# Performance work log

Measured on AMD Instinct MI355X. Metric: run time of the kernel, lower is better.

The kernel has to match this reference:

```python
import jax, jax.numpy as jnp
import numpy as np
from jax import lax

NUM_GROUPS = 16
POOL_K = 2
CLAMP_MIN = 0.0
CLAMP_MAX = 1.0
EPS = 1e-5


def setup_inputs() -> dict:
    key = jax.random.key(0)
    k1, k2, k3, k4, k5, k6 = jax.random.split(key, 6)
    B, Cin, H, W = 32, 64, 128, 128
    Cout, K = 128, 3
    x = jax.random.normal(k1, (B, Cin, H, W), dtype=jnp.float32)
    conv_w = jax.random.normal(k2, (Cout, Cin, K, K), dtype=jnp.float32) * 0.05
    conv_b = jax.random.normal(k3, (Cout,), dtype=jnp.float32) * 0.05
    gn_weight = jnp.ones((Cout,), dtype=jnp.float32) + 0.1 * jax.random.normal(k4, (Cout,), dtype=jnp.float32)
    gn_bias = 0.1 * jax.random.normal(k5, (Cout,), dtype=jnp.float32)
    scale = jnp.ones((Cout, 1, 1), dtype=jnp.float32) + 0.1 * jax.random.normal(k6, (Cout, 1, 1), dtype=jnp.float32)
    return {"x": x, "conv_w": conv_w, "conv_b": conv_b,
            "gn_weight": gn_weight, "gn_bias": gn_bias, "scale": scale}


def reference(x, conv_w, conv_b, gn_weight, gn_bias, scale):
    # Conv2d, VALID padding, stride 1  -> [B, C, H-2, W-2]
    y = lax.conv_general_dilated(
        x, conv_w, window_strides=(1, 1), padding='VALID',
        dimension_numbers=('NCHW', 'OIHW', 'NCHW'))
    y = y + conv_b[None, :, None, None]

    B, C, H, W = y.shape
    # GroupNorm: stats per (batch, group) over channels_per_group*H*W
    yg = y.reshape(B, NUM_GROUPS, -1)
    mean = jnp.mean(yg, axis=-1, keepdims=True)
    var = jnp.mean(jnp.square(yg - mean), axis=-1, keepdims=True)
    yn = ((yg - mean) * lax.rsqrt(var + EPS)).reshape(B, C, H, W)
    # affine + extra per-channel scale (fused elementwise)
    yn = (yn * gn_weight[None, :, None, None] + gn_bias[None, :, None, None]) * scale[None]

    # MaxPool2d(k=POOL_K), VALID, stride=k
    p = lax.reduce_window(yn, -jnp.inf, lax.max,
                          (1, 1, POOL_K, POOL_K), (1, 1, POOL_K, POOL_K), 'VALID')
    return jnp.clip(p, CLAMP_MIN, CLAMP_MAX)
```

## Files before the change

### kernel.cpp

```cpp
#include <hip/hip_runtime.h>

typedef _Float16 half8 __attribute__((ext_vector_type(8)));
typedef _Float16 half4t __attribute__((ext_vector_type(4)));
typedef _Float16 half2t __attribute__((ext_vector_type(2)));
typedef float float4t __attribute__((ext_vector_type(4)));

#define BATCH 32
#define CIN 64
#define HIN 128
#define WIN 128
#define COUT 128
#define HOUT 126
#define WOUT 126
#define YSTR 128
#define HP 63
#define WP 63
#define NGROUPS 16
#define CPG 8
#define EPSV 1e-5f

__global__ __launch_bounds__(256) void wt_kernel(const float* __restrict__ w,
                                                 _Float16* __restrict__ wT) {
    int idx = blockIdx.x * 256 + threadIdx.x;
    if (idx >= 9 * COUT * CIN) return;
    int cin = idx & 63;
    int t = idx >> 6;
    int cout = t & 127;
    int pos = t >> 7;
    wT[idx] = (_Float16)w[(cout * CIN + cin) * 9 + pos];
}

__global__ __launch_bounds__(256, 3) void conv_mfma_kernel(
    const float* __restrict__ x, const _Float16* __restrict__ wT,
    const float* __restrict__ bias, _Float16* __restrict__ yh,
    float* __restrict__ stats)
{
    __shared__ __align__(16) _Float16 xs[3 * 130 * 64];

    const int tid = threadIdx.x;
    int f = blockIdx.y * 126 + blockIdx.x;
    int w = (f & 7) * 504 + (f >> 3);
    const int oy = w % 126;
    const int b  = w / 126;

    {
        const int cp   = tid & 31;
        const int seg  = tid >> 5;
        const int c0   = 2 * cp;
        const int chk  = cp >> 2;
        const int wsub = (cp & 3) << 1;
        const float* xb = x + (size_t)b * CIN * (HIN * WIN);
        for (int i = 0; i < 12; i++) {
            int r = i >> 2;
            int col4 = seg * 16 + (i & 3) * 4;
            const float* p0 = xb + ((size_t)c0 * HIN + (oy + r)) * WIN + col4;
            const float* p1 = p0 + (size_t)HIN * WIN;
            float4t va = *(const float4t*)p0;
            float4t vb = *(const float4t*)p1;
            int Rb = r * 130 + col4;
#pragma unroll
            for (int j = 0; j < 4; j++) {
                int R = Rb + j;
                half2t hv = { (_Float16)va[j], (_Float16)vb[j] };
                *(half2t*)&xs[(R << 6) + ((chk ^ (R & 7)) << 3) + wsub] = hv;
            }
        }
        if (tid < 192) {
            int cpz = tid & 31;
            int R = (tid >> 6) * 130 + 128 + ((tid >> 5) & 1);
            half2t z = { (_Float16)0.f, (_Float16)0.f };
            *(half2t*)&xs[(R << 6) + (((cpz >> 2) ^ (R & 7)) << 3) + ((cpz & 3) << 1)] = z;
        }
    }
    __syncthreads();

    const int lane = tid & 63;
    const int wv   = tid >> 6;
    const int m    = lane & 15;
    const int q    = lane >> 4;
    const int cout0 = wv * 32;

    float4t acc[2][8];
#pragma unroll
    for (int s = 0; s < 2; s++)
#pragma unroll
        for (int n = 0; n < 8; n++)
            acc[s][n] = (float4t){0.f, 0.f, 0.f, 0.f};

    const _Float16* ab0 = wT + (size_t)(cout0 + m) * CIN + q * 8;
    half8 a0 = *(const half8*)(ab0);
    half8 a1 = *(const half8*)(ab0 + 16 * CIN);

    for (int kk = 0; kk < 18; kk++) {
        int pos = kk >> 1, ch = kk & 1;
        int kh = (pos > 2) + (pos > 5);
        int kw = pos - kh * 3;
        int R0 = kh * 130 + m + kw;
        const _Float16* bb = &xs[(R0 << 6) + (((q + 4 * ch) ^ (R0 & 7)) << 3)];

        half8 na0 = a0, na1 = a1;
        if (kk < 17) {
            int nk = kk + 1, npos = nk >> 1, nch = nk & 1;
            const _Float16* ab = wT + ((size_t)(npos * COUT + cout0 + m)) * CIN + q * 8 + nch * 32;
            na0 = *(const half8*)ab;
            na1 = *(const half8*)(ab + 16 * CIN);
        }
#pragma unroll
        for (int n = 0; n < 8; n++) {
            half8 bf = *(const half8*)(bb + n * 1024);
            acc[0][n] = __builtin_amdgcn_mfma_f32_16x16x32_f16(bf, a0, acc[0][n], 0, 0, 0);
            acc[1][n] = __builtin_amdgcn_mfma_f32_16x16x32_f16(bf, a1, acc[1][n], 0, 0, 0);
        }
        a0 = na0; a1 = na1;
    }

#pragma unroll
    for (int sub = 0; sub < 2; sub++) {
        const int c = cout0 + sub * 16 + m;
        const float bv = bias[c];
        _Float16* yrow = yh + (((size_t)b * COUT + c) * HOUT + oy) * YSTR;
        float sv = 0.f, ssv = 0.f;
#pragma unroll
        for (int n = 0; n < 8; n++) {
            int pix0 = n * 16 + q * 4;
            float v0 = acc[sub][n][0] + bv;
            float v1 = acc[sub][n][1] + bv;
            float v2 = acc[sub][n][2] + bv;
            float v3 = acc[sub][n][3] + bv;
            sv  += v0 + v1;
            ssv += v0 * v0 + v1 * v1;
            if (pix0 + 3 < WOUT) {
                sv  += v2 + v3;
                ssv += v2 * v2 + v3 * v3;
            }
            half4t hv = { (_Float16)v0, (_Float16)v1, (_Float16)v2, (_Float16)v3 };
            *(half4t*)(yrow + pix0) = hv;
        }
        sv  += __shfl_xor(sv, 1);   ssv += __shfl_xor(ssv, 1);
        sv  += __shfl_xor(sv, 2);   ssv += __shfl_xor(ssv, 2);
        sv  += __shfl_xor(sv, 4);   ssv += __shfl_xor(ssv, 4);
        sv  += __shfl_xor(sv, 16);  ssv += __shfl_xor(ssv, 16);
        sv  += __shfl_xor(sv, 32);  ssv += __shfl_xor(ssv, 32);
        if ((lane & 55) == 0) {
            int g = (cout0 >> 3) + sub * 2 + ((lane >> 3) & 1);
            atomicAdd(&stats[(b * NGROUPS + g) * 2 + 0], sv);
            atomicAdd(&stats[(b * NGROUPS + g) * 2 + 1], ssv);
        }
    }
}

__global__ __launch_bounds__(256) void norm_pool_kernel(
    const _Float16* __restrict__ yh, const float* __restrict__ stats,
    const float* __restrict__ gnw, const float* __restrict__ gnb,
    const float* __restrict__ scale, float* __restrict__ out)
{
    int idx = blockIdx.x * 256 + threadIdx.x;
    int wp = idx & 63;
    int hp = (idx >> 6) & 63;
    if (wp >= WP || hp >= HP) return;
    int c  = (idx >> 12) & 127;
    int b  = idx >> 19;

    const float N = (float)(CPG * HOUT * WOUT);
    int g = c >> 3;
    float sum   = stats[(b * NGROUPS + g) * 2 + 0];
    float sumsq = stats[(b * NGROUPS + g) * 2 + 1];
    float mean = sum / N;
    float var  = sumsq / N - mean * mean;
    float rstd = rsqrtf(var + EPSV);

    float gw = gnw[c] * rstd;
    float A  = gw * scale[c];
    float B2 = (gnb[c] - mean * gw) * scale[c];

    const _Float16* yp = yh + ((((size_t)b * COUT + c) * HOUT + hp * 2) << 7) + wp * 2;
    half2t r0 = *(const half2t*)yp;
    half2t r1 = *(const half2t*)(yp + YSTR);
    float v0 = fmaf((float)r0[0], A, B2);
    float v1 = fmaf((float)r0[1], A, B2);
    float v2 = fmaf((float)r1[0], A, B2);
    float v3 = fmaf((float)r1[1], A, B2);
    float mx = fmaxf(fmaxf(v0, v1), fmaxf(v2, v3));
    out[(((size_t)b * COUT + c) * HP + hp) * WP + wp] = fminf(fmaxf(mx, 0.0f), 1.0f);
}

extern "C" void kernel_launch(void* const* d_in, const int* in_sizes, int n_in,
                              void* d_out, int out_size, void* d_ws, size_t ws_size,
                              hipStream_t stream) {
    const float* x      = (const float*)d_in[0];
    const float* conv_w = (const float*)d_in[1];
    const float* conv_b = (const float*)d_in[2];
    const float* gnw    = (const float*)d_in[3];
    const float* gnb    = (const float*)d_in[4];
    const float* scale  = (const float*)d_in[5];
    float* out = (float*)d_out;

    const size_t y_bytes = (size_t)BATCH * COUT * HOUT * YSTR * sizeof(_Float16);
    _Float16* yh = (_Float16*)d_ws;
    float* stats = (float*)((char*)d_ws + y_bytes);
    _Float16* wT = (_Float16*)((char*)d_ws + y_bytes + 4096);

    hipMemsetAsync(stats, 0, BATCH * NGROUPS * 2 * sizeof(float), stream);

    wt_kernel<<<(9 * COUT * CIN + 255) / 256, 256, 0, stream>>>(conv_w, wT);

    dim3 grid(HOUT, BATCH);
    conv_mfma_kernel<<<grid, 256, 0, stream>>>(x, wT, conv_b, yh, stats);

    norm_pool_kernel<<<(BATCH * COUT * 64 * 64) / 256, 256, 0, stream>>>(
        yh, stats, gnw, gnb, scale, out);
}
```

Measured before the change: 401.4 us.

## Pre-repack input to swizzled fp16 NHWC and stream into LDS directly; vectorize pooling

A new repack kernel converts x once into a channel-last fp16 layout per row, already swizzled, so the conv kernel can copy three rows straight into LDS with global_load_lds. Before this, every conv block read and converted fp32 NCHW rows itself, which meant each input row was loaded three times with strided access. The norm/pool kernel now has each thread handle four outputs using 16-byte half8 loads and float4 stores. The cost is an extra kernel launch plus a round trip of the fp16 repacked input through workspace memory.

```diff
diff --git a/kernel.cpp b/kernel.cpp
--- a/kernel.cpp
+++ b/kernel.cpp
@@ -4,6 +4,7 @@
 typedef _Float16 half4t __attribute__((ext_vector_type(4)));
 typedef _Float16 half2t __attribute__((ext_vector_type(2)));
 typedef float float4t __attribute__((ext_vector_type(4)));
+typedef float float4u __attribute__((ext_vector_type(4), aligned(4)));
 
 #define BATCH 32
 #define CIN 64
@@ -19,6 +20,8 @@
 #define CPG 8
 #define EPSV 1e-5f
 
+#define XP_ROW 8320
+
 __global__ __launch_bounds__(256) void wt_kernel(const float* __restrict__ w,
                                                  _Float16* __restrict__ wT) {
     int idx = blockIdx.x * 256 + threadIdx.x;
@@ -30,12 +33,50 @@
     wT[idx] = (_Float16)w[(cout * CIN + cin) * 9 + pos];
 }
 
+__global__ __launch_bounds__(256) void repack_kernel(const float* __restrict__ x,
+                                                     _Float16* __restrict__ xp) {
+    __shared__ _Float16 lt[128 * 66];
+    const int tid = threadIdx.x;
+    const int grow = blockIdx.x;
+    const int b = blockIdx.y;
+
+    const int c0 = tid >> 5;
+    const int col0 = (tid & 31) * 4;
+#pragma unroll
+    for (int i = 0; i < 8; i++) {
+        int cin = c0 + 8 * i;
+        float4t v = *(const float4t*)(x + (((size_t)b * CIN + cin) * HIN + grow) * WIN + col0);
+#pragma unroll
+        for (int j = 0; j < 4; j++)
+            lt[(col0 + j) * 66 + cin] = (_Float16)v[j];
+    }
+    __syncthreads();
+
+    _Float16* xpb = xp + ((size_t)b * HIN + grow) * XP_ROW;
+#pragma unroll
+    for (int k = 0; k < 4; k++) {
+        int cidx = tid + 256 * k;
+        int col = cidx >> 3, chk = cidx & 7;
+        half8 v = *(const half8*)&lt[col * 66 + chk * 8];
+        int slot = chk ^ ((2 * grow + col) & 7);
+        *(half8*)(xpb + col * 64 + slot * 8) = v;
+    }
+    if (tid < 16) {
+        int col = 128 + (tid >> 3), chk = tid & 7;
+        int slot = chk ^ ((2 * grow + col) & 7);
+        half8 z;
+#pragma unroll
+        for (int j = 0; j < 8; j++) z[j] = (_Float16)0.f;
+        *(half8*)(xpb + col * 64 + slot * 8) = z;
+    }
+}
+
 __global__ __launch_bounds__(256, 3) void conv_mfma_kernel(
-    const float* __restrict__ x, const _Float16* __restrict__ wT,
+    const _Float16* __restrict__ xp, const _Float16* __restrict__ wT,
     const float* __restrict__ bias, _Float16* __restrict__ yh,
     float* __restrict__ stats)
 {
-    __shared__ __align__(16) _Float16 xs[3 * 130 * 64];
+    __shared__ __align__(16) _Float16 xs[25088];
 
     const int tid = threadIdx.x;
     int f = blockIdx.y * 126 + blockIdx.x;
@@ -43,42 +84,31 @@
     const int oy = w % 126;
     const int b  = w / 126;
 
-    {
-        const int cp   = tid & 31;
-        const int seg  = tid >> 5;
-        const int c0   = 2 * cp;
-        const int chk  = cp >> 2;
-        const int wsub = (cp & 3) << 1;
-        const float* xb = x + (size_t)b * CIN * (HIN * WIN);
-        for (int i = 0; i < 12; i++) {
-            int r = i >> 2;
-            int col4 = seg * 16 + (i & 3) * 4;
-            const float* p0 = xb + ((size_t)c0 * HIN + (oy + r)) * WIN + col4;
-            const float* p1 = p0 + (size_t)HIN * WIN;
-            float4t va = *(const float4t*)p0;
-            float4t vb = *(const float4t*)p1;
-            int Rb = r * 130 + col4;
-#pragma unroll
-            for (int j = 0; j < 4; j++) {
-                int R = Rb + j;
-                half2t hv = { (_Float16)va[j], (_Float16)vb[j] };
-                *(half2t*)&xs[(R << 6) + ((chk ^ (R & 7)) << 3) + wsub] = hv;
-            }
-        }
-        if (tid < 192) {
-            int cpz = tid & 31;
-            int R = (tid >> 6) * 130 + 128 + ((tid >> 5) & 1);
-            half2t z = { (_Float16)0.f, (_Float16)0.f };
-            *(half2t*)&xs[(R << 6) + (((cpz >> 2) ^ (R & 7)) << 3) + ((cpz & 3) << 1)] = z;
-        }
-    }
-    __syncthreads();
-
     const int lane = tid & 63;
     const int wv   = tid >> 6;
+
+    {
+        const char* src = (const char*)(xp + (size_t)(b * HIN + oy) * XP_ROW);
+        const int wb = wv * 1024;
+#pragma unroll
+        for (int k = 0; k < 12; k++) {
+            __builtin_amdgcn_global_load_lds(
+                (const __attribute__((address_space(1))) void*)(src + k * 4096 + wb + lane * 16),
+                (__attribute__((address_space(3))) void*)((char*)xs + k * 4096 + wb),
+                16, 0, 0);
+        }
+        if (wv == 0) {
+            __builtin_amdgcn_global_load_lds(
+                (const __attribute__((address_space(1))) void*)(src + 49152 + lane * 16),
+                (__attribute__((address_space(3))) void*)((char*)xs + 49152),
+                16, 0, 0);
+        }
+    }
+    __syncthreads();
+
     const int m    = lane & 15;
     const int q    = lane >> 4;
-    const int cout0 = wv * 32;
+    const int cout0 = (tid >> 6) * 32;
 
     float4t acc[2][8];
 #pragma unroll
@@ -95,8 +125,8 @@
         int pos = kk >> 1, ch = kk & 1;
         int kh = (pos > 2) + (pos > 5);
         int kw = pos - kh * 3;
-        int R0 = kh * 130 + m + kw;
-        const _Float16* bb = &xs[(R0 << 6) + (((q + 4 * ch) ^ (R0 & 7)) << 3)];
+        int key = (2 * (oy + kh) + m + kw) & 7;
+        const _Float16* bb = &xs[(kh * 130 + m + kw) * 64 + (((q + 4 * ch) ^ key) << 3)];
 
         half8 na0 = a0, na1 = a1;
         if (kk < 17) {
@@ -154,12 +184,12 @@
     const float* __restrict__ gnw, const float* __restrict__ gnb,
     const float* __restrict__ scale, float* __restrict__ out)
 {
-    int idx = blockIdx.x * 256 + threadIdx.x;
-    int wp = idx & 63;
-    int hp = (idx >> 6) & 63;
-    if (wp >= WP || hp >= HP) return;
-    int c  = (idx >> 12) & 127;
-    int b  = idx >> 19;
+    const int t  = threadIdx.x & 15;
+    const int hs = threadIdx.x >> 4;
+    const int hblk = blockIdx.x & 3;
+    const int c = (blockIdx.x >> 2) & 127;
+    const int b = blockIdx.x >> 9;
+    const int hp = hblk * 16 + hs;
 
     const float N = (float)(CPG * HOUT * WOUT);
     int g = c >> 3;
@@ -173,15 +203,29 @@
     float A  = gw * scale[c];
     float B2 = (gnb[c] - mean * gw) * scale[c];
 
-    const _Float16* yp = yh + ((((size_t)b * COUT + c) * HOUT + hp * 2) << 7) + wp * 2;
-    half2t r0 = *(const half2t*)yp;
-    half2t r1 = *(const half2t*)(yp + YSTR);
-    float v0 = fmaf((float)r0[0], A, B2);
-    float v1 = fmaf((float)r0[1], A, B2);
-    float v2 = fmaf((float)r1[0], A, B2);
-    float v3 = fmaf((float)r1[1], A, B2);
-    float mx = fmaxf(fmaxf(v0, v1), fmaxf(v2, v3));
-    out[(((size_t)b * COUT + c) * HP + hp) * WP + wp] = fminf(fmaxf(mx, 0.0f), 1.0f);
+    if (hp >= HP) return;
+
+    const _Float16* yp = yh + ((((size_t)b * COUT + c) * HOUT + hp * 2) << 7) + t * 8;
+    half8 r0 = *(const half8*)yp;
+    half8 r1 = *(const half8*)(yp + YSTR);
+
+    float o[4];
+#pragma unroll
+    for (int j = 0; j < 4; j++) {
+        float v0 = fmaf((float)r0[2 * j],     A, B2);
+        float v1 = fmaf((float)r0[2 * j + 1], A, B2);
+        float v2 = fmaf((float)r1[2 * j],     A, B2);
+        float v3 = fmaf((float)r1[2 * j + 1], A, B2);
+        float mx = fmaxf(fmaxf(v0, v1), fmaxf(v2, v3));
+        o[j] = fminf(fmaxf(mx, 0.0f), 1.0f);
+    }
+
+    float* op = out + (((size_t)b * COUT + c) * HP + hp) * WP + t * 4;
+    if (t < 15) {
+        *(float4u*)op = (float4u){o[0], o[1], o[2], o[3]};
+    } else {
+        op[0] = o[0]; op[1] = o[1]; op[2] = o[2];
+    }
 }
 
 extern "C" void kernel_launch(void* const* d_in, const int* in_sizes, int n_in,
@@ -199,14 +243,18 @@
     _Float16* yh = (_Float16*)d_ws;
     float* stats = (float*)((char*)d_ws + y_bytes);
     _Float16* wT = (_Float16*)((char*)d_ws + y_bytes + 4096);
+    _Float16* xp = (_Float16*)((char*)d_ws + y_bytes + 4096 + 147456);
 
     hipMemsetAsync(stats, 0, BATCH * NGROUPS * 2 * sizeof(float), stream);
 
     wt_kernel<<<(9 * COUT * CIN + 255) / 256, 256, 0, stream>>>(conv_w, wT);
 
+    dim3 rgrid(HIN, BATCH);
+    repack_kernel<<<rgrid, 256, 0, stream>>>(x, xp);
+
     dim3 grid(HOUT, BATCH);
-    conv_mfma_kernel<<<grid, 256, 0, stream>>>(x, wT, conv_b, yh, stats);
-
-    norm_pool_kernel<<<(BATCH * COUT * 64 * 64) / 256, 256, 0, stream>>>(
+    conv_mfma_kernel<<<grid, 256, 0, stream>>>(xp, wT, conv_b, yh, stats);
+
+    norm_pool_kernel<<<BATCH * COUT * 4, 256, 0, stream>>>(
         yh, stats, gnw, gnb, scale, out);
 }
```

After: 385.1 us. 4.1% less time.
